# Kernel tuning notes

Hardware: AMD Instinct MI355X
Metric: run time of the kernel (lower is better)

## Reference

```python
import jax, jax.numpy as jnp
import numpy as np

N_NODES = 100000
N_EDGES = 1600000
IN_FEATS, N_HIDDEN, N_CLASSES = 128, 128, 40


def _sage_layer(h, src, dst, W_self, W_neigh, b):
    # DGL SAGEConv (mean): fc_self(h) + fc_neigh(mean_{u in N_in(v)} h_u)
    msg = h[src]  # [E, F] gather of source-node features
    summed = jax.ops.segment_sum(msg, dst, num_segments=N_NODES)  # [N, F]
    deg = jax.ops.segment_sum(jnp.ones((src.shape[0], 1), h.dtype), dst,
                              num_segments=N_NODES)  # [N, 1] in-degree
    h_neigh = summed / jnp.maximum(deg, 1.0)
    return h @ W_self + b + h_neigh @ W_neigh


def setup_inputs() -> dict:
    key = jax.random.key(0)
    ks = jax.random.split(key, 12)
    inputs = jax.random.normal(ks[0], (N_NODES, IN_FEATS), dtype=jnp.float32)
    src = jax.random.randint(ks[1], (N_EDGES,), 0, N_NODES, dtype=jnp.int64)
    dst = jax.random.randint(ks[2], (N_EDGES,), 0, N_NODES, dtype=jnp.int64)

    def lin(k, fi, fo):
        return jax.random.normal(k, (fi, fo), dtype=jnp.float32) / np.sqrt(fi)

    return {
        "inputs": inputs, "src": src, "dst": dst,
        "W_self0": lin(ks[3], IN_FEATS, N_HIDDEN),
        "W_neigh0": lin(ks[4], IN_FEATS, N_HIDDEN),
        "b0": jnp.zeros((N_HIDDEN,), jnp.float32),
        "W_self1": lin(ks[5], N_HIDDEN, N_HIDDEN),
        "W_neigh1": lin(ks[6], N_HIDDEN, N_HIDDEN),
        "b1": jnp.zeros((N_HIDDEN,), jnp.float32),
        "W_self2": lin(ks[7], N_HIDDEN, N_CLASSES),
        "W_neigh2": lin(ks[8], N_HIDDEN, N_CLASSES),
        "b2": jnp.zeros((N_CLASSES,), jnp.float32),
    }


def reference(inputs, src, dst, W_self0, W_neigh0, b0, W_self1, W_neigh1, b1,
              W_self2, W_neigh2, b2):
    # dropout p=0.0 -> identity
    h = _sage_layer(inputs, src, dst, W_self0, W_neigh0, b0)
    h = jax.nn.relu(h)
    h = _sage_layer(h, src, dst, W_self1, W_neigh1, b1)
    h = jax.nn.relu(h)
    h = _sage_layer(h, src, dst, W_self2, W_neigh2, b2)
    return h
```

## Files before the change

kernel.cpp:

```cpp
#include <hip/hip_runtime.h>


#define F_IN 128
#define SCAN_CHUNK 1024

__global__ __launch_bounds__(256) void count_deg_kernel(
    const int* __restrict__ dst, int* __restrict__ cnt, int E) {
    int i = blockIdx.x * 256 + threadIdx.x;
    if (i < E) atomicAdd(&cnt[dst[i]], 1);
}

__global__ __launch_bounds__(256) void scan_part1(
    const int* __restrict__ cnt, int* __restrict__ bsum, int n) {
    __shared__ int red[4];
    int base = blockIdx.x * SCAN_CHUNK + threadIdx.x * 4;
    int s = 0;
    if (base + 4 <= n) {
        int4 v = *(const int4*)&cnt[base];
        s = v.x + v.y + v.z + v.w;
    } else {
        for (int j = 0; j < 4; ++j) if (base + j < n) s += cnt[base + j];
    }
    for (int off = 32; off > 0; off >>= 1) s += __shfl_down(s, off, 64);
    if ((threadIdx.x & 63) == 0) red[threadIdx.x >> 6] = s;
    __syncthreads();
    if (threadIdx.x == 0)
        bsum[blockIdx.x] = red[0] + red[1] + red[2] + red[3];
}

__global__ __launch_bounds__(256) void scan_part2(int* __restrict__ bsum, int nb) {
    __shared__ int tmp[256];
    int t = threadIdx.x;
    tmp[t] = (t < nb) ? bsum[t] : 0;
    __syncthreads();
    for (int off = 1; off < 256; off <<= 1) {
        int x = tmp[t];
        int add = (t >= off) ? tmp[t - off] : 0;
        __syncthreads();
        tmp[t] = x + add;
        __syncthreads();
    }
    if (t < nb) bsum[t] = (t == 0) ? 0 : tmp[t - 1];
}

__global__ __launch_bounds__(256) void scan_part3(
    const int* __restrict__ cnt, const int* __restrict__ bsum,
    int* __restrict__ row_ptr, int n, int E) {
    __shared__ int tsum[256];
    int t = threadIdx.x;
    int base = blockIdx.x * SCAN_CHUNK + t * 4;
    int c[4];
    int s = 0;
    #pragma unroll
    for (int j = 0; j < 4; ++j) {
        int idx = base + j;
        c[j] = (idx < n) ? cnt[idx] : 0;
        s += c[j];
    }
    tsum[t] = s;
    __syncthreads();
    for (int off = 1; off < 256; off <<= 1) {
        int x = tsum[t];
        int add = (t >= off) ? tsum[t - off] : 0;
        __syncthreads();
        tsum[t] = x + add;
        __syncthreads();
    }
    int p = bsum[blockIdx.x] + ((t == 0) ? 0 : tsum[t - 1]);
    #pragma unroll
    for (int j = 0; j < 4; ++j) {
        int idx = base + j;
        if (idx < n) { row_ptr[idx] = p; p += c[j]; }
    }
    if (blockIdx.x == 0 && t == 0) row_ptr[n] = E;
}

__global__ __launch_bounds__(256) void fill_kernel(
    const int* __restrict__ src, const int* __restrict__ dst,
    const int* __restrict__ row_ptr, int* __restrict__ cursor,
    int* __restrict__ col, int E) {
    int i = blockIdx.x * 256 + threadIdx.x;
    if (i < E) {
        int d = dst[i];
        int pos = atomicAdd(&cursor[d], 1);
        col[row_ptr[d] + pos] = src[i];
    }
}

__global__ __launch_bounds__(256) void aggregate_kernel(
    const float* __restrict__ h, const int* __restrict__ row_ptr,
    const int* __restrict__ col, float* __restrict__ hn, int n) {
    int g = (blockIdx.x * 256 + threadIdx.x) >> 5;
    int lane = threadIdx.x & 31;
    if (g >= n) return;
    int s = row_ptr[g], e = row_ptr[g + 1];
    const float4* h4 = (const float4*)h;
    float4 acc = make_float4(0.f, 0.f, 0.f, 0.f);
    int i = s;
    for (; i + 3 < e; i += 4) {
        int u0 = col[i], u1 = col[i + 1], u2 = col[i + 2], u3 = col[i + 3];
        float4 x0 = h4[(size_t)u0 * 32 + lane];
        float4 x1 = h4[(size_t)u1 * 32 + lane];
        float4 x2 = h4[(size_t)u2 * 32 + lane];
        float4 x3 = h4[(size_t)u3 * 32 + lane];
        acc.x += (x0.x + x1.x) + (x2.x + x3.x);
        acc.y += (x0.y + x1.y) + (x2.y + x3.y);
        acc.z += (x0.z + x1.z) + (x2.z + x3.z);
        acc.w += (x0.w + x1.w) + (x2.w + x3.w);
    }
    for (; i < e; ++i) {
        int u = col[i];
        float4 x = h4[(size_t)u * 32 + lane];
        acc.x += x.x; acc.y += x.y; acc.z += x.z; acc.w += x.w;
    }
    float inv = 1.f / fmaxf((float)(e - s), 1.f);
    float4 r = make_float4(acc.x * inv, acc.y * inv, acc.z * inv, acc.w * inv);
    ((float4*)hn)[(size_t)g * 32 + lane] = r;
}

template <int NTX, int RPT, int FO_PAD, bool RELU>
__global__ __launch_bounds__(256) void gemm_kernel(
    const float* __restrict__ A, const float* __restrict__ An,
    const float* __restrict__ Ws, const float* __restrict__ Wn,
    const float* __restrict__ b, float* __restrict__ out,
    int n, int fo_real) {
    constexpr int NTY = 256 / NTX;
    __shared__ float As[32][256];
    __shared__ float Wt[32][FO_PAD];

    int t = threadIdx.x;
    int block_row = blockIdx.x * 32;

    #pragma unroll
    for (int j = 0; j < 8; ++j) {
        int f = t + j * 256;
        int r = f >> 6, q = f & 63;
        int node = block_row + r;
        float4 v = make_float4(0.f, 0.f, 0.f, 0.f);
        if (node < n) {
            v = (q < 32) ? ((const float4*)A)[(size_t)node * 32 + q]
                         : ((const float4*)An)[(size_t)node * 32 + (q - 32)];
        }
        ((float4*)&As[r][0])[q] = v;
    }

    float acc[RPT][4];
    #pragma unroll
    for (int i = 0; i < RPT; ++i)
        for (int j = 0; j < 4; ++j) acc[i][j] = 0.f;

    int tx = t % NTX, ty = t / NTX;
    const int c0 = tx * 4;

    for (int kt = 0; kt < 8; ++kt) {
        __syncthreads();
        constexpr int F4 = (32 * FO_PAD / 4) / 256;
        #pragma unroll
        for (int j = 0; j < F4; ++j) {
            int f = t + j * 256;
            int kk = f / (FO_PAD / 4);
            int c4 = f % (FO_PAD / 4);
            int k = kt * 32 + kk;
            const float* Wrow = (k < 128) ? &Ws[(size_t)k * fo_real]
                                          : &Wn[(size_t)(k - 128) * fo_real];
            float4 v;
            if (fo_real == FO_PAD) {
                v = ((const float4*)Wrow)[c4];
            } else {
                int c = c4 * 4;
                v.x = (c + 0 < fo_real) ? Wrow[c + 0] : 0.f;
                v.y = (c + 1 < fo_real) ? Wrow[c + 1] : 0.f;
                v.z = (c + 2 < fo_real) ? Wrow[c + 2] : 0.f;
                v.w = (c + 3 < fo_real) ? Wrow[c + 3] : 0.f;
            }
            ((float4*)&Wt[kk][0])[c4] = v;
        }
        __syncthreads();

        #pragma unroll
        for (int kk = 0; kk < 32; kk += 4) {
            float4 a[RPT];
            #pragma unroll
            for (int i = 0; i < RPT; ++i)
                a[i] = *(const float4*)&As[ty * RPT + i][kt * 32 + kk];
            #pragma unroll
            for (int u = 0; u < 4; ++u) {
                float4 w = ((const float4*)&Wt[kk + u][0])[tx];
                #pragma unroll
                for (int i = 0; i < RPT; ++i) {
                    float av = (&a[i].x)[u];
                    acc[i][0] += av * w.x;
                    acc[i][1] += av * w.y;
                    acc[i][2] += av * w.z;
                    acc[i][3] += av * w.w;
                }
            }
        }
    }

    #pragma unroll
    for (int i = 0; i < RPT; ++i) {
        int node = block_row + ty * RPT + i;
        if (node >= n) continue;
        if (c0 + 4 <= fo_real) {
            float4 v;
            v.x = acc[i][0] + b[c0 + 0];
            v.y = acc[i][1] + b[c0 + 1];
            v.z = acc[i][2] + b[c0 + 2];
            v.w = acc[i][3] + b[c0 + 3];
            if (RELU) {
                v.x = fmaxf(v.x, 0.f); v.y = fmaxf(v.y, 0.f);
                v.z = fmaxf(v.z, 0.f); v.w = fmaxf(v.w, 0.f);
            }
            *(float4*)&out[(size_t)node * fo_real + c0] = v;
        } else {
            #pragma unroll
            for (int j = 0; j < 4; ++j) {
                int c = c0 + j;
                if (c < fo_real) {
                    float s = acc[i][j] + b[c];
                    if (RELU) s = fmaxf(s, 0.f);
                    out[(size_t)node * fo_real + c] = s;
                }
            }
        }
    }
}

static inline size_t align256(size_t x) { return (x + 255) & ~(size_t)255; }

extern "C" void kernel_launch(void* const* d_in, const int* in_sizes, int n_in,
                              void* d_out, int out_size, void* d_ws, size_t ws_size,
                              hipStream_t stream) {
    const float* inputs = (const float*)d_in[0];
    const int* src = (const int*)d_in[1];
    const int* dst = (const int*)d_in[2];
    const float* Ws0 = (const float*)d_in[3];
    const float* Wn0 = (const float*)d_in[4];
    const float* b0  = (const float*)d_in[5];
    const float* Ws1 = (const float*)d_in[6];
    const float* Wn1 = (const float*)d_in[7];
    const float* b1  = (const float*)d_in[8];
    const float* Ws2 = (const float*)d_in[9];
    const float* Wn2 = (const float*)d_in[10];
    const float* b2  = (const float*)d_in[11];

    const int N = in_sizes[0] / F_IN;
    const int E = in_sizes[1];

    char* ws = (char*)d_ws;
    size_t off = 0;
    size_t off_cnt    = off; off += align256((size_t)N * 4);
    size_t off_cursor = off; off += align256((size_t)N * 4);
    size_t zero_bytes = off;
    size_t off_rowptr = off; off += align256(((size_t)N + 1) * 4);
    size_t off_bsum   = off; off += align256(1024 * 4);
    size_t off_col    = off; off += align256((size_t)E * 4);
    size_t off_hneigh = off; off += align256((size_t)N * F_IN * 4);
    size_t off_bufA   = off; off += align256((size_t)N * F_IN * 4);
    size_t off_bufB   = off; off += align256((size_t)N * F_IN * 4);
    (void)ws_size;

    int*   cnt    = (int*)(ws + off_cnt);
    int*   cursor = (int*)(ws + off_cursor);
    int*   rowptr = (int*)(ws + off_rowptr);
    int*   bsum   = (int*)(ws + off_bsum);
    int*   col    = (int*)(ws + off_col);
    float* hneigh = (float*)(ws + off_hneigh);
    float* bufA   = (float*)(ws + off_bufA);
    float* bufB   = (float*)(ws + off_bufB);
    float* out    = (float*)d_out;

    hipMemsetAsync(ws, 0, zero_bytes, stream);

    int eb = (E + 255) / 256;
    int nb = (N + SCAN_CHUNK - 1) / SCAN_CHUNK;

    count_deg_kernel<<<eb, 256, 0, stream>>>(dst, cnt, E);
    scan_part1<<<nb, 256, 0, stream>>>(cnt, bsum, N);
    scan_part2<<<1, 256, 0, stream>>>(bsum, nb);
    scan_part3<<<nb, 256, 0, stream>>>(cnt, bsum, rowptr, N, E);
    fill_kernel<<<eb, 256, 0, stream>>>(src, dst, rowptr, cursor, col, E);

    int ab = (N * 32 + 255) / 256;
    int gb = (N + 31) / 32;

    aggregate_kernel<<<ab, 256, 0, stream>>>(inputs, rowptr, col, hneigh, N);
    gemm_kernel<32, 4, 128, true><<<gb, 256, 0, stream>>>(
        inputs, hneigh, Ws0, Wn0, b0, bufA, N, 128);

    aggregate_kernel<<<ab, 256, 0, stream>>>(bufA, rowptr, col, hneigh, N);
    gemm_kernel<32, 4, 128, true><<<gb, 256, 0, stream>>>(
        bufA, hneigh, Ws1, Wn1, b1, bufB, N, 128);

    aggregate_kernel<<<ab, 256, 0, stream>>>(bufB, rowptr, col, hneigh, N);
    gemm_kernel<16, 2, 64, false><<<gb, 256, 0, stream>>>(
        bufB, hneigh, Ws2, Wn2, b2, out, N, 40);
}
```

Before: 923.1 us.

## Replace FP32 SIMT GEMM with split-bf16 MFMA GEMM using pre-split weights

Replaces the shared-memory FP32 FMA GEMM with a kernel built on the 16x16x32 bf16 MFMA instruction. Weights are pre-transposed and split into hi/lo bf16 pairs by a small preprocessing kernel. Activations are split on the fly, and three MFMAs per tile (hi*hi, lo*hi, hi*lo) approximate FP32 accuracy. The aim is to cut the compute-bound dense GEMM time, at the cost of slightly lower precision, extra conversion ALU work, and uncoalesced scalar output stores.

Result: no change. 909.9 us (-1.4%).

```diff
diff --git a/kernel.cpp b/kernel.cpp
--- a/kernel.cpp
+++ b/kernel.cpp
@@ -3,6 +3,19 @@
 
 #define F_IN 128
 #define SCAN_CHUNK 1024
+
+typedef __attribute__((ext_vector_type(8))) short bf16x8;
+typedef __attribute__((ext_vector_type(4))) float f32x4;
+
+__device__ __forceinline__ unsigned short f32_to_bf16_rne(float x) {
+    unsigned int u = __float_as_uint(x);
+    unsigned int r = u + 0x7FFFu + ((u >> 16) & 1u);
+    return (unsigned short)(r >> 16);
+}
+__device__ __forceinline__ float bf16_bits_to_f32(unsigned short h) {
+    return __uint_as_float(((unsigned int)h) << 16);
+}
+
 
 __global__ __launch_bounds__(256) void count_deg_kernel(
     const int* __restrict__ dst, int* __restrict__ cnt, int E) {
@@ -118,110 +131,91 @@
     ((float4*)hn)[(size_t)g * 32 + lane] = r;
 }
 
-template <int NTX, int RPT, int FO_PAD, bool RELU>
-__global__ __launch_bounds__(256) void gemm_kernel(
+__global__ __launch_bounds__(256) void wsplit_kernel(
+    const float* __restrict__ Ws, const float* __restrict__ Wn,
+    unsigned short* __restrict__ hi, unsigned short* __restrict__ lo,
+    int fo, int fopad) {
+    int i = blockIdx.x * 256 + threadIdx.x;
+    if (i >= fopad * 256) return;
+    int c = i >> 8, k = i & 255;
+    float v = 0.f;
+    if (c < fo) v = (k < 128) ? Ws[(size_t)k * fo + c] : Wn[(size_t)(k - 128) * fo + c];
+    unsigned short h = f32_to_bf16_rne(v);
+    float hf = bf16_bits_to_f32(h);
+    unsigned short l = f32_to_bf16_rne(v - hf);
+    hi[i] = h; lo[i] = l;
+}
+
+template <int NT, bool RELU>
+__global__ __launch_bounds__(256) void gemm_mfma_kernel(
     const float* __restrict__ A, const float* __restrict__ An,
-    const float* __restrict__ Ws, const float* __restrict__ Wn,
-    const float* __restrict__ b, float* __restrict__ out,
-    int n, int fo_real) {
-    constexpr int NTY = 256 / NTX;
-    __shared__ float As[32][256];
-    __shared__ float Wt[32][FO_PAD];
-
-    int t = threadIdx.x;
-    int block_row = blockIdx.x * 32;
-
-    #pragma unroll
-    for (int j = 0; j < 8; ++j) {
-        int f = t + j * 256;
-        int r = f >> 6, q = f & 63;
-        int node = block_row + r;
-        float4 v = make_float4(0.f, 0.f, 0.f, 0.f);
-        if (node < n) {
-            v = (q < 32) ? ((const float4*)A)[(size_t)node * 32 + q]
-                         : ((const float4*)An)[(size_t)node * 32 + (q - 32)];
+    const unsigned short* __restrict__ Wt_hi,
+    const unsigned short* __restrict__ Wt_lo,
+    const float* __restrict__ bias, float* __restrict__ out,
+    int n, int fo) {
+    int wid  = threadIdx.x >> 6;
+    int lane = threadIdx.x & 63;
+    int r16  = lane & 15;
+    int kg   = lane >> 4;
+    int Rbase = blockIdx.x * 64 + wid * 16;
+
+    f32x4 acc[NT];
+    #pragma unroll
+    for (int ct = 0; ct < NT; ++ct) acc[ct] = (f32x4){0.f, 0.f, 0.f, 0.f};
+
+    int arow = Rbase + r16;
+    if (arow > n - 1) arow = n - 1;
+
+    #pragma unroll
+    for (int kstep = 0; kstep < 8; ++kstep) {
+        const float* srcp = (kstep < 4) ? A : An;
+        int koff = (kstep & 3) * 32 + kg * 8;
+        const float* p = srcp + (size_t)arow * F_IN + koff;
+        float4 v0 = *(const float4*)p;
+        float4 v1 = *(const float4*)(p + 4);
+
+        bf16x8 ahi, alo;
+        {
+            float va0 = v0.x, va1 = v0.y, va2 = v0.z, va3 = v0.w;
+            float va4 = v1.x, va5 = v1.y, va6 = v1.z, va7 = v1.w;
+            unsigned short h0 = f32_to_bf16_rne(va0), h1 = f32_to_bf16_rne(va1);
+            unsigned short h2 = f32_to_bf16_rne(va2), h3 = f32_to_bf16_rne(va3);
+            unsigned short h4 = f32_to_bf16_rne(va4), h5 = f32_to_bf16_rne(va5);
+            unsigned short h6 = f32_to_bf16_rne(va6), h7 = f32_to_bf16_rne(va7);
+            ahi[0] = (short)h0; ahi[1] = (short)h1; ahi[2] = (short)h2; ahi[3] = (short)h3;
+            ahi[4] = (short)h4; ahi[5] = (short)h5; ahi[6] = (short)h6; ahi[7] = (short)h7;
+            alo[0] = (short)f32_to_bf16_rne(va0 - bf16_bits_to_f32(h0));
+            alo[1] = (short)f32_to_bf16_rne(va1 - bf16_bits_to_f32(h1));
+            alo[2] = (short)f32_to_bf16_rne(va2 - bf16_bits_to_f32(h2));
+            alo[3] = (short)f32_to_bf16_rne(va3 - bf16_bits_to_f32(h3));
+            alo[4] = (short)f32_to_bf16_rne(va4 - bf16_bits_to_f32(h4));
+            alo[5] = (short)f32_to_bf16_rne(va5 - bf16_bits_to_f32(h5));
+            alo[6] = (short)f32_to_bf16_rne(va6 - bf16_bits_to_f32(h6));
+            alo[7] = (short)f32_to_bf16_rne(va7 - bf16_bits_to_f32(h7));
         }
-        ((float4*)&As[r][0])[q] = v;
-    }
-
-    float acc[RPT][4];
-    #pragma unroll
-    for (int i = 0; i < RPT; ++i)
-        for (int j = 0; j < 4; ++j) acc[i][j] = 0.f;
-
-    int tx = t % NTX, ty = t / NTX;
-    const int c0 = tx * 4;
-
-    for (int kt = 0; kt < 8; ++kt) {
-        __syncthreads();
-        constexpr int F4 = (32 * FO_PAD / 4) / 256;
+
+        int wkoff = kstep * 32 + kg * 8;
         #pragma unroll
-        for (int j = 0; j < F4; ++j) {
-            int f = t + j * 256;
-            int kk = f / (FO_PAD / 4);
-            int c4 = f % (FO_PAD / 4);
-            int k = kt * 32 + kk;
-            const float* Wrow = (k < 128) ? &Ws[(size_t)k * fo_real]
-                                          : &Wn[(size_t)(k - 128) * fo_real];
-            float4 v;
-            if (fo_real == FO_PAD) {
-                v = ((const float4*)Wrow)[c4];
-            } else {
-                int c = c4 * 4;
-                v.x = (c + 0 < fo_real) ? Wrow[c + 0] : 0.f;
-                v.y = (c + 1 < fo_real) ? Wrow[c + 1] : 0.f;
-                v.z = (c + 2 < fo_real) ? Wrow[c + 2] : 0.f;
-                v.w = (c + 3 < fo_real) ? Wrow[c + 3] : 0.f;
-            }
-            ((float4*)&Wt[kk][0])[c4] = v;
+        for (int ct = 0; ct < NT; ++ct) {
+            int c = ct * 16 + r16;
+            bf16x8 whi = *(const bf16x8*)(Wt_hi + (size_t)c * 256 + wkoff);
+            bf16x8 wlo = *(const bf16x8*)(Wt_lo + (size_t)c * 256 + wkoff);
+            acc[ct] = __builtin_amdgcn_mfma_f32_16x16x32_bf16(ahi, whi, acc[ct], 0, 0, 0);
+            acc[ct] = __builtin_amdgcn_mfma_f32_16x16x32_bf16(alo, whi, acc[ct], 0, 0, 0);
+            acc[ct] = __builtin_amdgcn_mfma_f32_16x16x32_bf16(ahi, wlo, acc[ct], 0, 0, 0);
         }
-        __syncthreads();
-
+    }
+
+    #pragma unroll
+    for (int ct = 0; ct < NT; ++ct) {
+        int c = ct * 16 + r16;
         #pragma unroll
-        for (int kk = 0; kk < 32; kk += 4) {
-            float4 a[RPT];
-            #pragma unroll
-            for (int i = 0; i < RPT; ++i)
-                a[i] = *(const float4*)&As[ty * RPT + i][kt * 32 + kk];
-            #pragma unroll
-            for (int u = 0; u < 4; ++u) {
-                float4 w = ((const float4*)&Wt[kk + u][0])[tx];
-                #pragma unroll
-                for (int i = 0; i < RPT; ++i) {
-                    float av = (&a[i].x)[u];
-                    acc[i][0] += av * w.x;
-                    acc[i][1] += av * w.y;
-                    acc[i][2] += av * w.z;
-                    acc[i][3] += av * w.w;
-                }
-            }
-        }
-    }
-
-    #pragma unroll
-    for (int i = 0; i < RPT; ++i) {
-        int node = block_row + ty * RPT + i;
-        if (node >= n) continue;
-        if (c0 + 4 <= fo_real) {
-            float4 v;
-            v.x = acc[i][0] + b[c0 + 0];
-            v.y = acc[i][1] + b[c0 + 1];
-            v.z = acc[i][2] + b[c0 + 2];
-            v.w = acc[i][3] + b[c0 + 3];
-            if (RELU) {
-                v.x = fmaxf(v.x, 0.f); v.y = fmaxf(v.y, 0.f);
-                v.z = fmaxf(v.z, 0.f); v.w = fmaxf(v.w, 0.f);
-            }
-            *(float4*)&out[(size_t)node * fo_real + c0] = v;
-        } else {
-            #pragma unroll
-            for (int j = 0; j < 4; ++j) {
-                int c = c0 + j;
-                if (c < fo_real) {
-                    float s = acc[i][j] + b[c];
-                    if (RELU) s = fmaxf(s, 0.f);
-                    out[(size_t)node * fo_real + c] = s;
-                }
+        for (int i = 0; i < 4; ++i) {
+            int node = Rbase + kg * 4 + i;
+            if (node < n && c < fo) {
+                float v = acc[ct][i] + bias[c];
+                if (RELU) v = fmaxf(v, 0.f);
+                out[(size_t)node * fo + c] = v;
             }
         }
     }
@@ -259,6 +253,12 @@
     size_t off_hneigh = off; off += align256((size_t)N * F_IN * 4);
     size_t off_bufA   = off; off += align256((size_t)N * F_IN * 4);
     size_t off_bufB   = off; off += align256((size_t)N * F_IN * 4);
+    size_t off_wt0h   = off; off += align256(128 * 256 * 2);
+    size_t off_wt0l   = off; off += align256(128 * 256 * 2);
+    size_t off_wt1h   = off; off += align256(128 * 256 * 2);
+    size_t off_wt1l   = off; off += align256(128 * 256 * 2);
+    size_t off_wt2h   = off; off += align256(48 * 256 * 2);
+    size_t off_wt2l   = off; off += align256(48 * 256 * 2);
     (void)ws_size;
 
     int*   cnt    = (int*)(ws + off_cnt);
@@ -269,6 +269,12 @@
     float* hneigh = (float*)(ws + off_hneigh);
     float* bufA   = (float*)(ws + off_bufA);
     float* bufB   = (float*)(ws + off_bufB);
+    unsigned short* wt0h = (unsigned short*)(ws + off_wt0h);
+    unsigned short* wt0l = (unsigned short*)(ws + off_wt0l);
+    unsigned short* wt1h = (unsigned short*)(ws + off_wt1h);
+    unsigned short* wt1l = (unsigned short*)(ws + off_wt1l);
+    unsigned short* wt2h = (unsigned short*)(ws + off_wt2h);
+    unsigned short* wt2l = (unsigned short*)(ws + off_wt2l);
     float* out    = (float*)d_out;
 
     hipMemsetAsync(ws, 0, zero_bytes, stream);
@@ -282,18 +288,22 @@
     scan_part3<<<nb, 256, 0, stream>>>(cnt, bsum, rowptr, N, E);
     fill_kernel<<<eb, 256, 0, stream>>>(src, dst, rowptr, cursor, col, E);
 
+    wsplit_kernel<<<(128 * 256) / 256, 256, 0, stream>>>(Ws0, Wn0, wt0h, wt0l, 128, 128);
+    wsplit_kernel<<<(128 * 256) / 256, 256, 0, stream>>>(Ws1, Wn1, wt1h, wt1l, 128, 128);
+    wsplit_kernel<<<(48 * 256) / 256, 256, 0, stream>>>(Ws2, Wn2, wt2h, wt2l, 40, 48);
+
     int ab = (N * 32 + 255) / 256;
-    int gb = (N + 31) / 32;
+    int gb = (N + 63) / 64;
 
     aggregate_kernel<<<ab, 256, 0, stream>>>(inputs, rowptr, col, hneigh, N);
-    gemm_kernel<32, 4, 128, true><<<gb, 256, 0, stream>>>(
-        inputs, hneigh, Ws0, Wn0, b0, bufA, N, 128);
+    gemm_mfma_kernel<8, true><<<gb, 256, 0, stream>>>(
+        inputs, hneigh, wt0h, wt0l, b0, bufA, N, 128);
 
     aggregate_kernel<<<ab, 256, 0, stream>>>(bufA, rowptr, col, hneigh, N);
-    gemm_kernel<32, 4, 128, true><<<gb, 256, 0, stream>>>(
-        bufA, hneigh, Ws1, Wn1, b1, bufB, N, 128);
+    gemm_mfma_kernel<8, true><<<gb, 256, 0, stream>>>(
+        bufA, hneigh, wt1h, wt1l, b1, bufB, N, 128);
 
     aggregate_kernel<<<ab, 256, 0, stream>>>(bufB, rowptr, col, hneigh, N);
-    gemm_kernel<16, 2, 64, false><<<gb, 256, 0, stream>>>(
-        bufB, hneigh, Ws2, Wn2, b2, out, N, 40);
-}
+    gemm_mfma_kernel<3, false><<<gb, 256, 0, stream>>>(
+        bufB, hneigh, wt2h, wt2l, b2, out, N, 40);
+}
```
